# Kernel optimization log

Measured on AMD Instinct MI355X. Metric: run time of the kernel, lower is better.

## Reference

```python
import jax, jax.numpy as jnp
import numpy as np

N_NODES = 50000
N_EDGES = 800000
IN_CH = 512
HID = 128
OUT_CH = 2
N_GRAPHS = 64
EPS = 1e-5


def _gcn_conv(x, src, dst, W, b):
    # GCNConv: out = D^-1/2 (A + I) D^-1/2 (x W) + b  (PyG semantics, self-loops added)
    n = x.shape[0]
    h = x @ W  # [N, H]
    loop = jnp.arange(n)
    src2 = jnp.concatenate([src, loop])
    dst2 = jnp.concatenate([dst, loop])
    deg = jax.ops.segment_sum(jnp.ones_like(dst2, dtype=h.dtype), dst2, num_segments=n)
    dinv = jax.lax.rsqrt(deg)  # deg >= 1 due to self-loops
    norm = dinv[src2] * dinv[dst2]  # [E+N]
    msg = h[src2] * norm[:, None]  # gather + normalize
    out = jax.ops.segment_sum(msg, dst2, num_segments=n)  # scatter-add
    return out + b


def _batchnorm_eval(x, gamma, beta, rm, rv):
    return (x - rm) * jax.lax.rsqrt(rv + EPS) * gamma + beta


def setup_inputs() -> dict:
    key = jax.random.key(0)
    ks = jax.random.split(key, 16)
    x = jax.random.normal(ks[0], (N_NODES, IN_CH), dtype=jnp.float32)
    edge_index = jax.random.randint(ks[1], (2, N_EDGES), 0, N_NODES, dtype=jnp.int64)
    batch = jnp.sort(jax.random.randint(ks[2], (N_NODES,), 0, N_GRAPHS, dtype=jnp.int64))
    s1 = 1.0 / np.sqrt(IN_CH)
    s2 = 1.0 / np.sqrt(HID)
    return {
        'x': x,
        'edge_index': edge_index,
        'batch': batch,
        'W1': jax.random.normal(ks[3], (IN_CH, HID), dtype=jnp.float32) * s1,
        'b1': jnp.zeros((HID,), dtype=jnp.float32),
        'gamma1': jax.random.normal(ks[4], (HID,), dtype=jnp.float32) * 0.1 + 1.0,
        'beta1': jax.random.normal(ks[5], (HID,), dtype=jnp.float32) * 0.1,
        'rm1': jax.random.normal(ks[6], (HID,), dtype=jnp.float32) * 0.1,
        'rv1': jax.random.uniform(ks[7], (HID,), dtype=jnp.float32, minval=0.5, maxval=1.5),
        'W2': jax.random.normal(ks[8], (HID, HID), dtype=jnp.float32) * s2,
        'b2': jnp.zeros((HID,), dtype=jnp.float32),
        'gamma2': jax.random.normal(ks[9], (HID,), dtype=jnp.float32) * 0.1 + 1.0,
        'beta2': jax.random.normal(ks[10], (HID,), dtype=jnp.float32) * 0.1,
        'rm2': jax.random.normal(ks[11], (HID,), dtype=jnp.float32) * 0.1,
        'rv2': jax.random.uniform(ks[12], (HID,), dtype=jnp.float32, minval=0.5, maxval=1.5),
        'Wl': jax.random.normal(ks[13], (HID, OUT_CH), dtype=jnp.float32) * s2,
        'bl': jnp.zeros((OUT_CH,), dtype=jnp.float32),
    }


def reference(x, edge_index, batch, W1, b1, gamma1, beta1, rm1, rv1,
              W2, b2, gamma2, beta2, rm2, rv2, Wl, bl):
    # Eval mode: BatchNorm uses running stats; dropout is identity.
    src, dst = edge_index[0], edge_index[1]
    h = _gcn_conv(x, src, dst, W1, b1)
    h = jax.nn.relu(_batchnorm_eval(h, gamma1, beta1, rm1, rv1))
    h = _gcn_conv(h, src, dst, W2, b2)
    h = jax.nn.relu(_batchnorm_eval(h, gamma2, beta2, rm2, rv2))
    # global mean pool over graphs in the batch
    sums = jax.ops.segment_sum(h, batch, num_segments=N_GRAPHS)  # [G, H]
    counts = jax.ops.segment_sum(jnp.ones((h.shape[0],), dtype=h.dtype), batch, num_segments=N_GRAPHS)
    pooled = sums / jnp.maximum(counts, 1.0)[:, None]
    return pooled @ Wl + bl  # [G, OUT_CH]
```

## Files before the change

kernel.cpp:

```cpp
#include <hip/hip_runtime.h>

#define EPSV 1e-5f

typedef __attribute__((ext_vector_type(8))) short short8;
typedef __attribute__((ext_vector_type(4))) float f32x4;
typedef unsigned int uint;
typedef unsigned short ushort;

__global__ __launch_bounds__(256) void init_k(int* __restrict__ cnt, int nnodes) {
    int i = blockIdx.x * 256 + threadIdx.x;
    if (i < nnodes) cnt[i] = 0;
}

__global__ __launch_bounds__(128) void gstart_k(const int* __restrict__ batch,
                                                int* __restrict__ gstart,
                                                int nnodes, int ngraphs) {
    int g = threadIdx.x;
    if (g > ngraphs) return;
    int lo = 0, hi = nnodes;
    while (lo < hi) {
        int mid = (lo + hi) >> 1;
        if (batch[mid] < g) lo = mid + 1; else hi = mid;
    }
    gstart[g] = lo;
}

__global__ __launch_bounds__(256) void degcount_k(const int* __restrict__ dst,
                                                  int* __restrict__ cnt,
                                                  int nedges) {
    int i = blockIdx.x * 256 + threadIdx.x;
    if (i < nedges) atomicAdd(&cnt[dst[i]], 1);
}

__global__ __launch_bounds__(256) void dinv_k(const int* __restrict__ cnt,
                                              float* __restrict__ dinv, int nnodes) {
    int i = blockIdx.x * 256 + threadIdx.x;
    if (i < nnodes) dinv[i] = rsqrtf(1.0f + (float)cnt[i]);
}

__global__ __launch_bounds__(256) void scan1_k(const int* __restrict__ cnt,
                                               int* __restrict__ rowptr,
                                               int* __restrict__ bsum, int n) {
    __shared__ int sh[256];
    const int tx = threadIdx.x;
    const int base = blockIdx.x * 1024;
    int v[4];
    int s = 0;
#pragma unroll
    for (int j = 0; j < 4; j++) {
        int idx = base + tx * 4 + j;
        v[j] = (idx < n) ? cnt[idx] : 0;
        s += v[j];
    }
    sh[tx] = s;
    __syncthreads();
#pragma unroll
    for (int off = 1; off < 256; off <<= 1) {
        int t = (tx >= off) ? sh[tx - off] : 0;
        __syncthreads();
        sh[tx] += t;
        __syncthreads();
    }
    int run = sh[tx] - s;
#pragma unroll
    for (int j = 0; j < 4; j++) {
        int idx = base + tx * 4 + j;
        if (idx < n) rowptr[idx] = run;
        run += v[j];
    }
    if (tx == 255) bsum[blockIdx.x] = sh[255];
}

__global__ __launch_bounds__(64) void scan2_k(int* __restrict__ bsum, int nb) {
    __shared__ int sh[64];
    const int tx = threadIdx.x;
    int v = (tx < nb) ? bsum[tx] : 0;
    sh[tx] = v;
    __syncthreads();
#pragma unroll
    for (int off = 1; off < 64; off <<= 1) {
        int t = (tx >= off) ? sh[tx - off] : 0;
        __syncthreads();
        sh[tx] += t;
        __syncthreads();
    }
    if (tx < nb) bsum[tx] = sh[tx] - v;
}

__global__ __launch_bounds__(256) void scan3_k(int* __restrict__ rowptr,
                                               int* __restrict__ cur,
                                               const int* __restrict__ bsum,
                                               int n, int nedges) {
    const int tx = threadIdx.x;
    const int base = blockIdx.x * 1024;
    int off = bsum[blockIdx.x];
#pragma unroll
    for (int j = 0; j < 4; j++) {
        int idx = base + tx * 4 + j;
        if (idx < n) {
            int r = rowptr[idx] + off;
            rowptr[idx] = r;
            cur[idx] = r;
        }
    }
    if (blockIdx.x == 0 && tx == 0) rowptr[n] = nedges;
}

__global__ __launch_bounds__(256) void fill_k(const int* __restrict__ src,
                                              const int* __restrict__ dst,
                                              int* __restrict__ cur,
                                              int* __restrict__ esrc, int nedges) {
    int i = blockIdx.x * 256 + threadIdx.x;
    if (i >= nedges) return;
    int pos = atomicAdd(&cur[dst[i]], 1);
    esrc[pos] = src[i];
}

template <int K>
__global__ __launch_bounds__(256) void wprep_k(const float* __restrict__ W,
                                               ushort* __restrict__ wT) {
    int i = blockIdx.x * 256 + threadIdx.x;
    if (i >= K * 128) return;
    int k = i >> 7, c = i & 127;
    unsigned u = __builtin_bit_cast(unsigned, W[i]);
    wT[c * K + k] = (ushort)((u + 0x7fffu + ((u >> 16) & 1u)) >> 16);
}

template <int K>
__global__ __launch_bounds__(256) void gemm_mfma_k(const float* __restrict__ X,
                                                   const ushort* __restrict__ wT,
                                                   const float* __restrict__ dinv,
                                                   float* __restrict__ H,
                                                   ushort* __restrict__ hb16,
                                                   int nrows) {
    __shared__ ushort bsm[3][8192];

    const int tx = threadIdx.x;
    const int wu = __builtin_amdgcn_readfirstlane(tx >> 6);
    const int l = tx & 63;
    const int lrow = l & 15;
    const int kgrp = l >> 4;
    const int row0 = blockIdx.x * 64 + wu * 16;

    const ushort* sp[4];
#pragma unroll
    for (int q = 0; q < 4; q++) {
        int chunk = (wu * 4 + q) * 64 + l;
        int c = chunk >> 3;
        int s = (chunk & 7) ^ (c & 7);
        sp[q] = wT + (size_t)c * K + s * 8;
    }

    int arow = row0 + lrow;
    if (arow >= nrows) arow = nrows - 1;
    const float* xrow = X + (size_t)arow * K + kgrp * 8;

    f32x4 acc[8];
#pragma unroll
    for (int g = 0; g < 8; g++) acc[g] = (f32x4){0.f, 0.f, 0.f, 0.f};

    auto STAGE = [&](int buf, int k0) {
#pragma unroll
        for (int q = 0; q < 4; q++) {
            const ushort* src = sp[q] + k0;
            ushort* dst = &bsm[buf][(wu * 4 + q) * 512];
            __builtin_amdgcn_global_load_lds(
                (const __attribute__((address_space(1))) unsigned int*)(const void*)src,
                (__attribute__((address_space(3))) unsigned int*)(void*)dst,
                16, 0, 0);
        }
    };

    constexpr int NIT = K / 64;

    STAGE(0, 0);
    STAGE(1, 64);
    asm volatile("" ::: "memory");
    f32x4 c0 = *reinterpret_cast<const f32x4*>(xrow);
    f32x4 c1 = *reinterpret_cast<const f32x4*>(xrow + 4);
    f32x4 c2 = *reinterpret_cast<const f32x4*>(xrow + 32);
    f32x4 c3 = *reinterpret_cast<const f32x4*>(xrow + 36);

#pragma unroll
    for (int i = 0; i < NIT; i++) {
        if (i + 1 < NIT) asm volatile("s_waitcnt vmcnt(8)" ::: "memory");
        else             asm volatile("s_waitcnt vmcnt(0)" ::: "memory");
        __builtin_amdgcn_s_barrier();
        __builtin_amdgcn_sched_barrier(0);

        f32x4 n0 = c0, n1 = c1, n2 = c2, n3 = c3;
        if (i + 1 < NIT) {
            const float* nx = xrow + (i + 1) * 64;
            n0 = *reinterpret_cast<const f32x4*>(nx);
            n1 = *reinterpret_cast<const f32x4*>(nx + 4);
            n2 = *reinterpret_cast<const f32x4*>(nx + 32);
            n3 = *reinterpret_cast<const f32x4*>(nx + 36);
        }

        const ushort* b = bsm[i % 3];
#pragma unroll
        for (int sub = 0; sub < 2; sub++) {
            short8 ah, al;
#pragma unroll
            for (int j = 0; j < 8; j++) {
                float f = (sub == 0) ? ((j < 4) ? c0[j] : c1[j - 4])
                                     : ((j < 4) ? c2[j] : c3[j - 4]);
                unsigned u = __builtin_bit_cast(unsigned, f);
                ah[j] = (short)(u >> 16);
                float hif = __builtin_bit_cast(float, u & 0xffff0000u);
                float lof = f - hif;
                al[j] = (short)(__builtin_bit_cast(unsigned, lof) >> 16);
            }
#pragma unroll
            for (int g = 0; g < 8; g++) {
                int c = g * 16 + lrow;
                int phys = (sub * 4 + kgrp) ^ (c & 7);
                short8 bb = *reinterpret_cast<const short8*>(&b[c * 64 + phys * 8]);
                acc[g] = __builtin_amdgcn_mfma_f32_16x16x32_bf16(ah, bb, acc[g], 0, 0, 0);
                acc[g] = __builtin_amdgcn_mfma_f32_16x16x32_bf16(al, bb, acc[g], 0, 0, 0);
            }
        }

        asm volatile("" ::: "memory");
        if (i + 2 < NIT) STAGE((i + 2) % 3, (i + 2) * 64);
        asm volatile("" ::: "memory");

        c0 = n0; c1 = n1; c2 = n2; c3 = n3;
    }

#pragma unroll
    for (int r = 0; r < 4; r++) {
        int row = row0 + kgrp * 4 + r;
        if (row < nrows) {
            float dn = dinv[row];
            float* hrow = H + (size_t)row * 128 + lrow;
            ushort* hbrow = hb16 + (size_t)row * 128 + lrow;
#pragma unroll
            for (int g = 0; g < 8; g++) {
                float v = acc[g][r];
                hrow[g * 16] = v;
                unsigned u = __builtin_bit_cast(unsigned, v * dn);
                hbrow[g * 16] = (ushort)((u + 0x7fffu + ((u >> 16) & 1u)) >> 16);
            }
        }
    }
}

__global__ __launch_bounds__(256) void agg_k(const float* __restrict__ H,
                                             const uint* __restrict__ hb,
                                             const int* __restrict__ rowptr,
                                             const int* __restrict__ esrc,
                                             const float* __restrict__ dinv,
                                             const float* __restrict__ bias,
                                             const float* __restrict__ gamma,
                                             const float* __restrict__ beta,
                                             const float* __restrict__ rm,
                                             const float* __restrict__ rv,
                                             float* __restrict__ OUT,
                                             int nnodes) {
    int node = blockIdx.x * 4 + (threadIdx.x >> 6);
    if (node >= nnodes) return;
    node = __builtin_amdgcn_readfirstlane(node);
    const int l = threadIdx.x & 63;
    const int c = l * 2;
    const float dn = dinv[node];
    const int beg = rowptr[node], end = rowptr[node + 1];

    float2 hv = *reinterpret_cast<const float2*>(H + (size_t)node * 128 + c);
    float ax0 = hv.x * dn, ay0 = hv.y * dn;
    float ax1 = 0.f, ay1 = 0.f, ax2 = 0.f, ay2 = 0.f, ax3 = 0.f, ay3 = 0.f;
    const uint* hbl = hb + l;

    int j = beg;
    for (; j + 3 < end; j += 4) {
        int s0 = esrc[j], s1 = esrc[j + 1], s2 = esrc[j + 2], s3 = esrc[j + 3];
        uint u0 = hbl[(size_t)s0 * 64];
        uint u1 = hbl[(size_t)s1 * 64];
        uint u2 = hbl[(size_t)s2 * 64];
        uint u3 = hbl[(size_t)s3 * 64];
        ax0 += __builtin_bit_cast(float, u0 << 16);
        ay0 += __builtin_bit_cast(float, u0 & 0xffff0000u);
        ax1 += __builtin_bit_cast(float, u1 << 16);
        ay1 += __builtin_bit_cast(float, u1 & 0xffff0000u);
        ax2 += __builtin_bit_cast(float, u2 << 16);
        ay2 += __builtin_bit_cast(float, u2 & 0xffff0000u);
        ax3 += __builtin_bit_cast(float, u3 << 16);
        ay3 += __builtin_bit_cast(float, u3 & 0xffff0000u);
    }
    for (; j < end; j++) {
        uint u0 = hbl[(size_t)esrc[j] * 64];
        ax0 += __builtin_bit_cast(float, u0 << 16);
        ay0 += __builtin_bit_cast(float, u0 & 0xffff0000u);
    }
    float accx = (ax0 + ax1) + (ax2 + ax3);
    float accy = (ay0 + ay1) + (ay2 + ay3);

    float v0 = accx * dn + bias[c];
    float v1 = accy * dn + bias[c + 1];
    v0 = (v0 - rm[c])     * rsqrtf(rv[c] + EPSV)     * gamma[c]     + beta[c];
    v1 = (v1 - rm[c + 1]) * rsqrtf(rv[c + 1] + EPSV) * gamma[c + 1] + beta[c + 1];
    v0 = fmaxf(v0, 0.0f);
    v1 = fmaxf(v1, 0.0f);

    *reinterpret_cast<float2*>(OUT + (size_t)node * 128 + c) = make_float2(v0, v1);
}

__global__ __launch_bounds__(256) void pool1_k(const float* __restrict__ V,
                                               const int* __restrict__ gstart,
                                               float* __restrict__ partial) {
    __shared__ float sh[256];
    const int g = blockIdx.x >> 5;
    const int p = blockIdx.x & 31;
    const int tx = threadIdx.x;
    const int ch = tx & 127;
    const int sub = tx >> 7;
    const int beg = gstart[g], end = gstart[g + 1];
    const int chunk = (end - beg + 31) >> 5;
    const int s = beg + p * chunk;
    const int e = min(s + chunk, end);
    float acc = 0.0f;
    for (int i = s + sub; i < e; i += 2)
        acc += V[(size_t)i * 128 + ch];
    sh[tx] = acc;
    __syncthreads();
    if (tx < 128)
        partial[(size_t)blockIdx.x * 128 + tx] = sh[tx] + sh[tx + 128];
}

__global__ __launch_bounds__(128) void pool2_k(const float* __restrict__ partial,
                                               const int* __restrict__ gstart,
                                               float* __restrict__ pooled) {
    const int g = blockIdx.x;
    const int ch = threadIdx.x;
    float s = 0.0f;
#pragma unroll
    for (int p = 0; p < 32; p++)
        s += partial[(size_t)((g << 5) + p) * 128 + ch];
    float cnt = fmaxf((float)(gstart[g + 1] - gstart[g]), 1.0f);
    pooled[g * 128 + ch] = s / cnt;
}

__global__ __launch_bounds__(128) void final_k(const float* __restrict__ pooled,
                                               const float* __restrict__ Wl,
                                               const float* __restrict__ bl,
                                               float* __restrict__ out) {
    int tx = threadIdx.x;
    int g = tx >> 1, o = tx & 1;
    float s = 0.0f;
#pragma unroll 8
    for (int c = 0; c < 128; c++) s += pooled[g * 128 + c] * Wl[c * 2 + o];
    out[tx] = s + bl[o];
}

extern "C" void kernel_launch(void* const* d_in, const int* in_sizes, int n_in,
                              void* d_out, int out_size, void* d_ws, size_t ws_size,
                              hipStream_t stream) {
    const float* x      = (const float*)d_in[0];
    const int*   ei     = (const int*)d_in[1];
    const int*   batch  = (const int*)d_in[2];
    const float* W1     = (const float*)d_in[3];
    const float* b1     = (const float*)d_in[4];
    const float* gamma1 = (const float*)d_in[5];
    const float* beta1  = (const float*)d_in[6];
    const float* rm1    = (const float*)d_in[7];
    const float* rv1    = (const float*)d_in[8];
    const float* W2     = (const float*)d_in[9];
    const float* b2     = (const float*)d_in[10];
    const float* gamma2 = (const float*)d_in[11];
    const float* beta2  = (const float*)d_in[12];
    const float* rm2    = (const float*)d_in[13];
    const float* rv2    = (const float*)d_in[14];
    const float* Wl     = (const float*)d_in[15];
    const float* bl     = (const float*)d_in[16];
    float* out = (float*)d_out;

    const int nnodes  = in_sizes[2];
    const int nedges  = in_sizes[1] / 2;
    const int ngraphs = 64;
    const int* srcp = ei;
    const int* dstp = ei + nedges;

    float* wsA     = (float*)d_ws;
    float* wsB     = wsA + (size_t)nnodes * 128;
    float* dinv    = wsB + (size_t)nnodes * 128;
    float* pooled  = dinv + nnodes;
    float* partial = pooled + 64 * 128;
    int*   cnt     = (int*)(partial + 64 * 32 * 128);
    int*   rowptr  = cnt + nnodes;
    int*   cur     = rowptr + nnodes + 1;
    int*   bsum    = cur + nnodes;
    int*   gstart  = bsum + 64;
    int*   esrc    = gstart + 65;
    uintptr_t wp   = ((uintptr_t)(esrc + nedges) + 15) & ~(uintptr_t)15;
    ushort* wt1  = (ushort*)wp;
    ushort* wt2  = wt1 + 512 * 128;
    ushort* hb16 = wt2 + 128 * 128;
    uint*   hb   = (uint*)hb16;

    dim3 blk(256);
    const int gNodes = (nnodes + 255) / 256;
    const int gEdges = (nedges + 255) / 256;
    const int gGemm  = (nnodes + 63) / 64;
    const int gAgg   = (nnodes + 3) / 4;
    const int nScanB = (nnodes + 1023) / 1024;

    init_k<<<gNodes, blk, 0, stream>>>(cnt, nnodes);
    gstart_k<<<1, 128, 0, stream>>>(batch, gstart, nnodes, ngraphs);
    wprep_k<512><<<(512 * 128) / 256, blk, 0, stream>>>(W1, wt1);
    wprep_k<128><<<(128 * 128) / 256, blk, 0, stream>>>(W2, wt2);
    degcount_k<<<gEdges, blk, 0, stream>>>(dstp, cnt, nedges);
    dinv_k<<<gNodes, blk, 0, stream>>>(cnt, dinv, nnodes);
    scan1_k<<<nScanB, blk, 0, stream>>>(cnt, rowptr, bsum, nnodes);
    scan2_k<<<1, 64, 0, stream>>>(bsum, nScanB);
    scan3_k<<<nScanB, blk, 0, stream>>>(rowptr, cur, bsum, nnodes, nedges);
    fill_k<<<gEdges, blk, 0, stream>>>(srcp, dstp, cur, esrc, nedges);

    gemm_mfma_k<512><<<gGemm, blk, 0, stream>>>(x, wt1, dinv, wsA, hb16, nnodes);
    agg_k<<<gAgg, blk, 0, stream>>>(wsA, hb, rowptr, esrc, dinv, b1, gamma1, beta1,
                                    rm1, rv1, wsB, nnodes);

    gemm_mfma_k<128><<<gGemm, blk, 0, stream>>>(wsB, wt2, dinv, wsA, hb16, nnodes);
    agg_k<<<gAgg, blk, 0, stream>>>(wsA, hb, rowptr, esrc, dinv, b2, gamma2, beta2,
                                    rm2, rv2, wsB, nnodes);

    pool1_k<<<ngraphs * 32, blk, 0, stream>>>(wsB, gstart, partial);
    pool2_k<<<ngraphs, 128, 0, stream>>>(partial, gstart, pooled);
    final_k<<<1, 128, 0, stream>>>(pooled, Wl, bl, out);
}
```

Before: 258.4 us.

## Fuse small setup kernels and retile GEMM to 32-row blocks with 2-way column split

```diff
diff --git a/kernel.cpp b/kernel.cpp
--- a/kernel.cpp
+++ b/kernel.cpp
@@ -7,22 +7,21 @@
 typedef unsigned int uint;
 typedef unsigned short ushort;
 
-__global__ __launch_bounds__(256) void init_k(int* __restrict__ cnt, int nnodes) {
+__global__ __launch_bounds__(256) void init_k(int* __restrict__ cnt,
+                                              const int* __restrict__ batch,
+                                              int* __restrict__ gstart,
+                                              int nnodes, int ngraphs) {
     int i = blockIdx.x * 256 + threadIdx.x;
     if (i < nnodes) cnt[i] = 0;
-}
-
-__global__ __launch_bounds__(128) void gstart_k(const int* __restrict__ batch,
-                                                int* __restrict__ gstart,
-                                                int nnodes, int ngraphs) {
-    int g = threadIdx.x;
-    if (g > ngraphs) return;
-    int lo = 0, hi = nnodes;
-    while (lo < hi) {
-        int mid = (lo + hi) >> 1;
-        if (batch[mid] < g) lo = mid + 1; else hi = mid;
-    }
-    gstart[g] = lo;
+    if (blockIdx.x == 0 && threadIdx.x <= ngraphs) {
+        int g = threadIdx.x;
+        int lo = 0, hi = nnodes;
+        while (lo < hi) {
+            int mid = (lo + hi) >> 1;
+            if (batch[mid] < g) lo = mid + 1; else hi = mid;
+        }
+        gstart[g] = lo;
+    }
 }
 
 __global__ __launch_bounds__(256) void degcount_k(const int* __restrict__ dst,
@@ -32,15 +31,10 @@
     if (i < nedges) atomicAdd(&cnt[dst[i]], 1);
 }
 
-__global__ __launch_bounds__(256) void dinv_k(const int* __restrict__ cnt,
-                                              float* __restrict__ dinv, int nnodes) {
-    int i = blockIdx.x * 256 + threadIdx.x;
-    if (i < nnodes) dinv[i] = rsqrtf(1.0f + (float)cnt[i]);
-}
-
 __global__ __launch_bounds__(256) void scan1_k(const int* __restrict__ cnt,
                                                int* __restrict__ rowptr,
-                                               int* __restrict__ bsum, int n) {
+                                               int* __restrict__ bsum,
+                                               float* __restrict__ dinv, int n) {
     __shared__ int sh[256];
     const int tx = threadIdx.x;
     const int base = blockIdx.x * 1024;
@@ -50,6 +44,7 @@
     for (int j = 0; j < 4; j++) {
         int idx = base + tx * 4 + j;
         v[j] = (idx < n) ? cnt[idx] : 0;
+        if (idx < n) dinv[idx] = rsqrtf(1.0f + (float)v[j]);
         s += v[j];
     }
     sh[tx] = s;
@@ -116,14 +111,21 @@
     esrc[pos] = src[i];
 }
 
-template <int K>
-__global__ __launch_bounds__(256) void wprep_k(const float* __restrict__ W,
-                                               ushort* __restrict__ wT) {
+__global__ __launch_bounds__(256) void wprep_k(const float* __restrict__ W1,
+                                               const float* __restrict__ W2,
+                                               ushort* __restrict__ wt1,
+                                               ushort* __restrict__ wt2) {
     int i = blockIdx.x * 256 + threadIdx.x;
-    if (i >= K * 128) return;
-    int k = i >> 7, c = i & 127;
-    unsigned u = __builtin_bit_cast(unsigned, W[i]);
-    wT[c * K + k] = (ushort)((u + 0x7fffu + ((u >> 16) & 1u)) >> 16);
+    if (i < 512 * 128) {
+        int k = i >> 7, c = i & 127;
+        unsigned u = __builtin_bit_cast(unsigned, W1[i]);
+        wt1[c * 512 + k] = (ushort)((u + 0x7fffu + ((u >> 16) & 1u)) >> 16);
+    } else if (i < 512 * 128 + 128 * 128) {
+        int j = i - 512 * 128;
+        int k = j >> 7, c = j & 127;
+        unsigned u = __builtin_bit_cast(unsigned, W2[j]);
+        wt2[c * 128 + k] = (ushort)((u + 0x7fffu + ((u >> 16) & 1u)) >> 16);
+    }
 }
 
 template <int K>
@@ -133,14 +135,16 @@
                                                    float* __restrict__ H,
                                                    ushort* __restrict__ hb16,
                                                    int nrows) {
-    __shared__ ushort bsm[3][8192];
+    __shared__ ushort bsm[2][8192];
 
     const int tx = threadIdx.x;
     const int wu = __builtin_amdgcn_readfirstlane(tx >> 6);
     const int l = tx & 63;
     const int lrow = l & 15;
     const int kgrp = l >> 4;
-    const int row0 = blockIdx.x * 64 + wu * 16;
+    const int wrow = wu >> 1;
+    const int wcol = wu & 1;
+    const int row0 = blockIdx.x * 32 + wrow * 16;
 
     const ushort* sp[4];
 #pragma unroll
@@ -155,9 +159,9 @@
     if (arow >= nrows) arow = nrows - 1;
     const float* xrow = X + (size_t)arow * K + kgrp * 8;
 
-    f32x4 acc[8];
-#pragma unroll
-    for (int g = 0; g < 8; g++) acc[g] = (f32x4){0.f, 0.f, 0.f, 0.f};
+    f32x4 acc[4];
+#pragma unroll
+    for (int g = 0; g < 4; g++) acc[g] = (f32x4){0.f, 0.f, 0.f, 0.f};
 
     auto STAGE = [&](int buf, int k0) {
 #pragma unroll
@@ -174,30 +178,40 @@
     constexpr int NIT = K / 64;
 
     STAGE(0, 0);
-    STAGE(1, 64);
     asm volatile("" ::: "memory");
     f32x4 c0 = *reinterpret_cast<const f32x4*>(xrow);
     f32x4 c1 = *reinterpret_cast<const f32x4*>(xrow + 4);
     f32x4 c2 = *reinterpret_cast<const f32x4*>(xrow + 32);
     f32x4 c3 = *reinterpret_cast<const f32x4*>(xrow + 36);
+    f32x4 d0 = c0, d1 = c1, d2 = c2, d3 = c3;
+    if (NIT > 1) {
+        d0 = *reinterpret_cast<const f32x4*>(xrow + 64);
+        d1 = *reinterpret_cast<const f32x4*>(xrow + 68);
+        d2 = *reinterpret_cast<const f32x4*>(xrow + 96);
+        d3 = *reinterpret_cast<const f32x4*>(xrow + 100);
+    }
 
 #pragma unroll
     for (int i = 0; i < NIT; i++) {
-        if (i + 1 < NIT) asm volatile("s_waitcnt vmcnt(8)" ::: "memory");
-        else             asm volatile("s_waitcnt vmcnt(0)" ::: "memory");
+        if (i == 0 && NIT > 1)   asm volatile("s_waitcnt vmcnt(8)" ::: "memory");
+        else if (i + 1 < NIT)    asm volatile("s_waitcnt vmcnt(4)" ::: "memory");
+        else                     asm volatile("s_waitcnt vmcnt(0)" ::: "memory");
         __builtin_amdgcn_s_barrier();
         __builtin_amdgcn_sched_barrier(0);
 
-        f32x4 n0 = c0, n1 = c1, n2 = c2, n3 = c3;
-        if (i + 1 < NIT) {
-            const float* nx = xrow + (i + 1) * 64;
-            n0 = *reinterpret_cast<const f32x4*>(nx);
-            n1 = *reinterpret_cast<const f32x4*>(nx + 4);
-            n2 = *reinterpret_cast<const f32x4*>(nx + 32);
-            n3 = *reinterpret_cast<const f32x4*>(nx + 36);
-        }
-
-        const ushort* b = bsm[i % 3];
+        if (i + 1 < NIT) STAGE((i + 1) & 1, (i + 1) * 64);
+        asm volatile("" ::: "memory");
+
+        f32x4 e0 = d0, e1 = d1, e2 = d2, e3 = d3;
+        if (i + 2 < NIT) {
+            const float* nx = xrow + (i + 2) * 64;
+            e0 = *reinterpret_cast<const f32x4*>(nx);
+            e1 = *reinterpret_cast<const f32x4*>(nx + 4);
+            e2 = *reinterpret_cast<const f32x4*>(nx + 32);
+            e3 = *reinterpret_cast<const f32x4*>(nx + 36);
+        }
+
+        const ushort* b = bsm[i & 1];
 #pragma unroll
         for (int sub = 0; sub < 2; sub++) {
             short8 ah, al;
@@ -212,20 +226,17 @@
                 al[j] = (short)(__builtin_bit_cast(unsigned, lof) >> 16);
             }
 #pragma unroll
-            for (int g = 0; g < 8; g++) {
-                int c = g * 16 + lrow;
-                int phys = (sub * 4 + kgrp) ^ (c & 7);
-                short8 bb = *reinterpret_cast<const short8*>(&b[c * 64 + phys * 8]);
+            for (int g = 0; g < 4; g++) {
+                int cc = (wcol * 4 + g) * 16 + lrow;
+                int phys = (sub * 4 + kgrp) ^ (cc & 7);
+                short8 bb = *reinterpret_cast<const short8*>(&b[cc * 64 + phys * 8]);
                 acc[g] = __builtin_amdgcn_mfma_f32_16x16x32_bf16(ah, bb, acc[g], 0, 0, 0);
                 acc[g] = __builtin_amdgcn_mfma_f32_16x16x32_bf16(al, bb, acc[g], 0, 0, 0);
             }
         }
 
-        asm volatile("" ::: "memory");
-        if (i + 2 < NIT) STAGE((i + 2) % 3, (i + 2) * 64);
-        asm volatile("" ::: "memory");
-
-        c0 = n0; c1 = n1; c2 = n2; c3 = n3;
+        c0 = d0; c1 = d1; c2 = d2; c3 = d3;
+        d0 = e0; d1 = e1; d2 = e2; d3 = e3;
     }
 
 #pragma unroll
@@ -233,10 +244,10 @@
         int row = row0 + kgrp * 4 + r;
         if (row < nrows) {
             float dn = dinv[row];
-            float* hrow = H + (size_t)row * 128 + lrow;
-            ushort* hbrow = hb16 + (size_t)row * 128 + lrow;
-#pragma unroll
-            for (int g = 0; g < 8; g++) {
+            float* hrow = H + (size_t)row * 128 + wcol * 64 + lrow;
+            ushort* hbrow = hb16 + (size_t)row * 128 + wcol * 64 + lrow;
+#pragma unroll
+            for (int g = 0; g < 4; g++) {
                 float v = acc[g][r];
                 hrow[g * 16] = v;
                 unsigned u = __builtin_bit_cast(unsigned, v * dn);
@@ -400,17 +411,14 @@
     dim3 blk(256);
     const int gNodes = (nnodes + 255) / 256;
     const int gEdges = (nedges + 255) / 256;
-    const int gGemm  = (nnodes + 63) / 64;
+    const int gGemm  = (nnodes + 31) / 32;
     const int gAgg   = (nnodes + 3) / 4;
     const int nScanB = (nnodes + 1023) / 1024;
 
-    init_k<<<gNodes, blk, 0, stream>>>(cnt, nnodes);
-    gstart_k<<<1, 128, 0, stream>>>(batch, gstart, nnodes, ngraphs);
-    wprep_k<512><<<(512 * 128) / 256, blk, 0, stream>>>(W1, wt1);
-    wprep_k<128><<<(128 * 128) / 256, blk, 0, stream>>>(W2, wt2);
+    init_k<<<gNodes, blk, 0, stream>>>(cnt, batch, gstart, nnodes, ngraphs);
+    wprep_k<<<(512 * 128 + 128 * 128 + 255) / 256, blk, 0, stream>>>(W1, W2, wt1, wt2);
     degcount_k<<<gEdges, blk, 0, stream>>>(dstp, cnt, nedges);
-    dinv_k<<<gNodes, blk, 0, stream>>>(cnt, dinv, nnodes);
-    scan1_k<<<nScanB, blk, 0, stream>>>(cnt, rowptr, bsum, nnodes);
+    scan1_k<<<nScanB, blk, 0, stream>>>(cnt, rowptr, bsum, dinv, nnodes);
     scan2_k<<<1, 64, 0, stream>>>(bsum, nScanB);
     scan3_k<<<nScanB, blk, 0, stream>>>(rowptr, cur, bsum, nnodes, nedges);
     fill_k<<<gEdges, blk, 0, stream>>>(srcp, dstp, cur, esrc, nedges);
```

Result: slower. 263.8 us (+2.1%).
